# Performance work log

Measured on AMD Instinct MI355X. Metric: run time of the kernel, lower is better.

Reference implementation:

```python
import jax, jax.numpy as jnp
import numpy as np

N_HEAD = 16
D_K = 64


def _bn(x, g, b, eps=1e-5):
    # torch BatchNorm1d in training mode: biased batch variance
    m = jnp.mean(x, axis=0)
    v = jnp.var(x, axis=0)
    return (x - m) * jax.lax.rsqrt(v + eps) * g + b


def setup_inputs() -> dict:
    key = jax.random.key(0)
    ks = jax.random.split(key, 8)
    B, DX, NK, DKIN, H, DK, DO = 128, 1024, 1024, 512, N_HEAD, D_K, 512
    sc = 0.02
    return {
        "x": jax.random.normal(ks[0], (B, DX), dtype=jnp.float32),
        "k": jax.random.normal(ks[1], (B, NK, DKIN), dtype=jnp.float32),
        "bn1_g": jnp.ones((DX,), jnp.float32),
        "bn1_b": jnp.zeros((DX,), jnp.float32),
        "Wx": jax.random.normal(ks[2], (H * DK, DX), dtype=jnp.float32) * sc,
        "bx": jnp.zeros((H * DK,), jnp.float32),
        "Wk": jax.random.normal(ks[3], (H * DK, DKIN), dtype=jnp.float32) * sc,
        "bk": jnp.zeros((H * DK,), jnp.float32),
        "bn2_g": jnp.ones((DK,), jnp.float32),
        "bn2_b": jnp.zeros((DK,), jnp.float32),
        "Wlin": jax.random.normal(ks[4], (DK, DK), dtype=jnp.float32) * sc,
        "blin": jnp.zeros((DK,), jnp.float32),
        "Wo": jax.random.normal(ks[5], (DO, H * DK), dtype=jnp.float32) * sc,
        "bo": jnp.zeros((DO,), jnp.float32),
    }


def reference(x, k, bn1_g, bn1_b, Wx, bx, Wk, bk, bn2_g, bn2_b, Wlin, blin, Wo, bo):
    H, DK = N_HEAD, D_K
    B, DX = x.shape
    NK = k.shape[1]
    # outer BN + query projection (n_x == 1)
    xq = _bn(x, bn1_g, bn1_b) @ Wx.T + bx                     # (B, H*DK)
    xq = xq.reshape(B, H, DK).transpose(1, 0, 2).reshape(H * B, DK)
    kp = (k @ Wk.T + bk).reshape(B, NK, H, DK)
    kp = kp.transpose(2, 0, 1, 3).reshape(H * B, NK, DK)       # (H*B, NK, DK)
    # inner CrossAttention: BN + linear on the single query vector
    latent = _bn(xq, bn2_g, bn2_b) @ Wlin.T + blin             # (H*B, DK)
    u = jnp.einsum('bnd,bd->bn', kp, latent)                   # (H*B, NK)
    # softmax over the singleton query dim (dim=2) -> all ones, kept faithful
    attn = jax.nn.softmax(u[..., None], axis=-1)[..., 0]       # (H*B, NK)
    out = jnp.einsum('bnd,bn->bd', kp, attn)                   # (H*B, DK)
    out = out.reshape(H, B, DK).transpose(1, 0, 2).reshape(B, H * DK)
    x_hid = latent.reshape(H, B, DK).transpose(1, 0, 2).reshape(B, H * DK)
    # attn.view(n_head, batch, d_x_).permute(1,2,0).contiguous().view(batch, n_head, -1)
    attn_out = attn.reshape(H, B, NK).transpose(1, 2, 0).reshape(B, H, -1)
    return (attn_out, out @ Wo.T + bo, x_hid @ Wo.T + bo)
```

## Files before the change

### kernel.cpp

```cpp
#include <hip/hip_runtime.h>

typedef __attribute__((ext_vector_type(8))) short short8;
typedef __attribute__((ext_vector_type(4))) float floatx4;

__device__ __forceinline__ unsigned short f2bf(float f) {
    unsigned int x = __float_as_uint(f);
    x = x + 0x7FFFu + ((x >> 16) & 1u);
    return (unsigned short)(x >> 16);
}

template <typename OutT>
__device__ __forceinline__ void gemm_tile(
    const unsigned short* __restrict__ A, int lda,
    const unsigned short* __restrict__ B, int ldb,
    const float* __restrict__ bias, float bscale,
    OutT* __restrict__ C, int ldc, int tilesN, int K, int wave, int lane)
{
    int tm = wave / tilesN, tn = wave % tilesN;
    int mn = lane & 15, q = lane >> 4;
    const short8* ap = (const short8*)(A + (size_t)(tm * 16 + mn) * lda + q * 8);
    const short8* bp = (const short8*)(B + (size_t)(tn * 16 + mn) * ldb + q * 8);
    floatx4 acc = {0.f, 0.f, 0.f, 0.f};
    #pragma unroll 4
    for (int k = 0; k < K; k += 32) {
        short8 a = *ap; ap += 4;
        short8 b = *bp; bp += 4;
        acc = __builtin_amdgcn_mfma_f32_16x16x32_bf16(a, b, acc, 0, 0, 0);
    }
    int col = tn * 16 + mn;
    float bv = bias[col] * bscale;
    #pragma unroll
    for (int r = 0; r < 4; ++r) {
        int row = tm * 16 + q * 4 + r;
        float v = acc[r] + bv;
        OutT* dst = C + (size_t)row * ldc + col;
        if constexpr (sizeof(OutT) == 2) *dst = (OutT)f2bf(v);
        else                             *dst = (OutT)v;
    }
}

__global__ __launch_bounds__(256) void k_mega(
    const float* __restrict__ kk, float* __restrict__ part,
    const float* __restrict__ Wx, const float* __restrict__ Wk,
    const float* __restrict__ Wo, const float* __restrict__ Wl,
    unsigned short* __restrict__ Wxbf, unsigned short* __restrict__ Wkbf,
    unsigned short* __restrict__ Wobf, unsigned short* __restrict__ Wlbf,
    float4* __restrict__ attn_out,
    const float* __restrict__ x, const float* __restrict__ g1,
    const float* __restrict__ b1, unsigned short* __restrict__ xnbf)
{
    int blk = blockIdx.x, tid = threadIdx.x;
    if (blk < 1024) {
        int b = blk >> 3, c = blk & 7;
        int f4 = tid & 127;
        int rh = tid >> 7;
        const float4* base = (const float4*)kk
            + ((size_t)(b * 1024 + c * 128 + rh) * 128 + f4);
        float4 acc = {0.f, 0.f, 0.f, 0.f};
        #pragma unroll 8
        for (int it = 0; it < 64; ++it) {
            float4 v = base[(size_t)it * 256];
            acc.x += v.x; acc.y += v.y; acc.z += v.z; acc.w += v.w;
        }
        __shared__ float red[2][512];
        red[rh][f4 * 4 + 0] = acc.x;
        red[rh][f4 * 4 + 1] = acc.y;
        red[rh][f4 * 4 + 2] = acc.z;
        red[rh][f4 * 4 + 3] = acc.w;
        __syncthreads();
        for (int j = tid; j < 512; j += 256)
            part[((size_t)(c * 128 + b) << 9) + j] = red[0][j] + red[1][j];
    } else if (blk < 3076) {
        int f = (blk - 1024) * 256 + tid;
        const float* src; unsigned short* dst; int off;
        if (f < 262144)      { src = Wx; dst = Wxbf; off = f; }
        else if (f < 393216) { src = Wk; dst = Wkbf; off = f - 262144; }
        else if (f < 524288) { src = Wo; dst = Wobf; off = f - 393216; }
        else                 { src = Wl; dst = Wlbf; off = f - 524288; }
        float4 v = ((const float4*)src)[off];
        uint2 o;
        o.x = (unsigned int)f2bf(v.x) | ((unsigned int)f2bf(v.y) << 16);
        o.y = (unsigned int)f2bf(v.z) | ((unsigned int)f2bf(v.w) << 16);
        *(uint2*)(dst + off * 4) = o;
    } else if (blk < 5124) {
        int idx = (blk - 3076) * 256 + tid;
        float4 ones = {1.f, 1.f, 1.f, 1.f};
        attn_out[idx] = ones;
    } else {
        int c = (blk - 5124) * 256 + tid;
        float s = 0.f, ss = 0.f;
        #pragma unroll 8
        for (int b = 0; b < 128; ++b) {
            float v = x[b * 1024 + c];
            s += v; ss += v * v;
        }
        float m  = s * (1.f / 128.f);
        float va = ss * (1.f / 128.f) - m * m;
        float rs = rsqrtf(va + 1e-5f);
        float a  = rs * g1[c];
        float b2 = b1[c] - m * a;
        #pragma unroll 8
        for (int b = 0; b < 128; ++b)
            xnbf[b * 1024 + c] = f2bf(x[b * 1024 + c] * a + b2);
    }
}

__global__ __launch_bounds__(256) void k_combine_xq(
    const float* __restrict__ part, unsigned short* __restrict__ ksumbf,
    const unsigned short* __restrict__ xnbf, const unsigned short* __restrict__ Wxbf,
    const float* __restrict__ bx, float* __restrict__ xq)
{
    int blk = blockIdx.x, tid = threadIdx.x;
    if (blk < 32) {
        int idx = blk * 256 + tid;
        int b = idx >> 6;
        int j0 = (idx & 63) * 8;
        float s[8];
        #pragma unroll
        for (int u = 0; u < 8; ++u) s[u] = 0.f;
        #pragma unroll
        for (int c = 0; c < 8; ++c) {
            const float4* p = (const float4*)(part + ((size_t)(c * 128 + b) << 9) + j0);
            float4 a0 = p[0], a1 = p[1];
            s[0] += a0.x; s[1] += a0.y; s[2] += a0.z; s[3] += a0.w;
            s[4] += a1.x; s[5] += a1.y; s[6] += a1.z; s[7] += a1.w;
        }
        uint4 v;
        v.x = (unsigned int)f2bf(s[0]) | ((unsigned int)f2bf(s[1]) << 16);
        v.y = (unsigned int)f2bf(s[2]) | ((unsigned int)f2bf(s[3]) << 16);
        v.z = (unsigned int)f2bf(s[4]) | ((unsigned int)f2bf(s[5]) << 16);
        v.w = (unsigned int)f2bf(s[6]) | ((unsigned int)f2bf(s[7]) << 16);
        *(uint4*)(ksumbf + b * 512 + j0) = v;
    } else {
        int wave = ((blk - 32) * 256 + tid) >> 6;
        gemm_tile<float>(xnbf, 1024, Wxbf, 1024, bx, 1.f, xq, 1024, 64, 1024,
                         wave, tid & 63);
    }
}

__global__ __launch_bounds__(256) void k_bn2_outf(
    const float* __restrict__ xq, const float* __restrict__ g2,
    const float* __restrict__ b2, float* __restrict__ ab,
    const unsigned short* __restrict__ ksumbf, const unsigned short* __restrict__ Wkbf,
    const float* __restrict__ bk, unsigned short* __restrict__ concat)
{
    int blk = blockIdx.x, tid = threadIdx.x;
    if (blk < 64) {
        int d = blk;
        float s = 0.f, ss = 0.f;
        for (int e = tid; e < 2048; e += 256) {
            int b = e >> 4, h = e & 15;
            float v = xq[b * 1024 + h * 64 + d];
            s += v; ss += v * v;
        }
        __shared__ float r1[256], r2[256];
        r1[tid] = s; r2[tid] = ss;
        __syncthreads();
        for (int off = 128; off; off >>= 1) {
            if (tid < off) { r1[tid] += r1[tid + off]; r2[tid] += r2[tid + off]; }
            __syncthreads();
        }
        if (tid == 0) {
            float m  = r1[0] * (1.f / 2048.f);
            float va = r2[0] * (1.f / 2048.f) - m * m;
            float rs = rsqrtf(va + 1e-5f);
            float a  = rs * g2[d];
            ab[d] = a;
            ab[64 + d] = b2[d] - m * a;
        }
    } else {
        int wave = ((blk - 64) * 256 + tid) >> 6;
        gemm_tile<unsigned short>(ksumbf, 512, Wkbf, 512, bk, 1024.f, concat,
                                  1024, 64, 512, wave, tid & 63);
    }
}

__global__ __launch_bounds__(256) void k_latent(
    const float* __restrict__ xq, const float* __restrict__ ab,
    const unsigned short* __restrict__ Wlbf, const float* __restrict__ bl,
    unsigned short* __restrict__ xhid)
{
    int tid = threadIdx.x;
    int r = tid >> 6, dp = tid & 63;
    int row = blockIdx.x * 4 + r;
    int h = row >> 7, b = row & 127;
    __shared__ float xs[4][64];
    xs[r][dp] = xq[b * 1024 + h * 64 + dp] * ab[dp] + ab[64 + dp];
    __syncthreads();
    float dot = bl[dp];
    #pragma unroll 16
    for (int d = 0; d < 64; ++d)
        dot += xs[r][d] * __uint_as_float(((unsigned int)Wlbf[dp * 64 + d]) << 16);
    xhid[b * 1024 + h * 64 + dp] = f2bf(dot);
}

__global__ __launch_bounds__(256) void k_final_gemm(
    const unsigned short* __restrict__ concat, const unsigned short* __restrict__ Wobf,
    const float* __restrict__ bo, float* __restrict__ out12)
{
    int wave = (blockIdx.x * 256 + threadIdx.x) >> 6;
    gemm_tile<float>(concat, 1024, Wobf, 1024, bo, 1.f, out12, 512, 32, 1024,
                     wave, threadIdx.x & 63);
}

extern "C" void kernel_launch(void* const* d_in, const int* in_sizes, int n_in,
                              void* d_out, int out_size, void* d_ws, size_t ws_size,
                              hipStream_t stream) {
    (void)in_sizes; (void)n_in; (void)out_size; (void)ws_size;
    const float* x  = (const float*)d_in[0];
    const float* kk = (const float*)d_in[1];
    const float* g1 = (const float*)d_in[2];
    const float* b1 = (const float*)d_in[3];
    const float* Wx = (const float*)d_in[4];
    const float* bx = (const float*)d_in[5];
    const float* Wk = (const float*)d_in[6];
    const float* bk = (const float*)d_in[7];
    const float* g2 = (const float*)d_in[8];
    const float* b2 = (const float*)d_in[9];
    const float* Wl = (const float*)d_in[10];
    const float* bl = (const float*)d_in[11];
    const float* Wo = (const float*)d_in[12];
    const float* bo = (const float*)d_in[13];

    char* ws = (char*)d_ws;
    float*          part   = (float*)(ws + 0);
    unsigned short* Wxbf   = (unsigned short*)(ws + 2097152);
    unsigned short* Wkbf   = (unsigned short*)(ws + 4194304);
    unsigned short* Wobf   = (unsigned short*)(ws + 5242880);
    unsigned short* Wlbf   = (unsigned short*)(ws + 6291456);
    unsigned short* xnbf   = (unsigned short*)(ws + 6299648);
    unsigned short* ksumbf = (unsigned short*)(ws + 6561792);
    float*          xq     = (float*)(ws + 6692864);
    float*          ab     = (float*)(ws + 7217152);
    unsigned short* concat = (unsigned short*)(ws + 7217664);
    float*          out12  = (float*)d_out + 2097152;

    k_mega<<<5128, 256, 0, stream>>>(kk, part, Wx, Wk, Wo, Wl,
                                     Wxbf, Wkbf, Wobf, Wlbf,
                                     (float4*)d_out, x, g1, b1, xnbf);
    k_combine_xq<<<160, 256, 0, stream>>>(part, ksumbf, xnbf, Wxbf, bx, xq);
    k_bn2_outf<<<192, 256, 0, stream>>>(xq, g2, b2, ab, ksumbf, Wkbf, bk, concat);
    k_latent<<<512, 256, 0, stream>>>(xq, ab, Wlbf, bl, concat + 131072);
    k_final_gemm<<<128, 256, 0, stream>>>(concat, Wobf, bo, out12);
}
```

Baseline: 425.2 us.

## Fuse BN2 statistics into xq GEMM epilogue and merge latent MFMA with out-projection

The per-column BN2 sum and sum-of-squares are now accumulated with shared-memory and global atomics in the xq GEMM epilogue, which removes the separate reduction pass over xq. The latent linear layer moves onto MFMA and shares one launch with the Wk GEMM, so the pipeline has four launches instead of five. Block sizes drop to 128 threads with more blocks to spread the small GEMMs across more CUs. The cost is atomic contention and a float summation order that is no longer deterministic.

```diff
diff --git a/kernel.cpp b/kernel.cpp
--- a/kernel.cpp
+++ b/kernel.cpp
@@ -9,12 +9,13 @@
     return (unsigned short)(x >> 16);
 }
 
-template <typename OutT>
+template <typename OutT, bool STATS>
 __device__ __forceinline__ void gemm_tile(
     const unsigned short* __restrict__ A, int lda,
     const unsigned short* __restrict__ B, int ldb,
     const float* __restrict__ bias, float bscale,
-    OutT* __restrict__ C, int ldc, int tilesN, int K, int wave, int lane)
+    OutT* __restrict__ C, int ldc, int tilesN, int K, int wave, int lane,
+    float* sS, float* sSS)
 {
     int tm = wave / tilesN, tn = wave % tilesN;
     int mn = lane & 15, q = lane >> 4;
@@ -29,6 +30,7 @@
     }
     int col = tn * 16 + mn;
     float bv = bias[col] * bscale;
+    float lsum = 0.f, lss = 0.f;
     #pragma unroll
     for (int r = 0; r < 4; ++r) {
         int row = tm * 16 + q * 4 + r;
@@ -36,6 +38,12 @@
         OutT* dst = C + (size_t)row * ldc + col;
         if constexpr (sizeof(OutT) == 2) *dst = (OutT)f2bf(v);
         else                             *dst = (OutT)v;
+        if constexpr (STATS) { lsum += v; lss += v * v; }
+    }
+    if constexpr (STATS) {
+        int d = col & 63;
+        atomicAdd(&sS[d], lsum);
+        atomicAdd(&sSS[d], lss);
     }
 }
 
@@ -47,7 +55,8 @@
     unsigned short* __restrict__ Wobf, unsigned short* __restrict__ Wlbf,
     float4* __restrict__ attn_out,
     const float* __restrict__ x, const float* __restrict__ g1,
-    const float* __restrict__ b1, unsigned short* __restrict__ xnbf)
+    const float* __restrict__ b1, unsigned short* __restrict__ xnbf,
+    float* __restrict__ stats)
 {
     int blk = blockIdx.x, tid = threadIdx.x;
     if (blk < 1024) {
@@ -87,6 +96,7 @@
         float4 ones = {1.f, 1.f, 1.f, 1.f};
         attn_out[idx] = ones;
     } else {
+        if (blk == 5124 && tid < 128) stats[tid] = 0.f;
         int c = (blk - 5124) * 256 + tid;
         float s = 0.f, ss = 0.f;
         #pragma unroll 8
@@ -105,14 +115,15 @@
     }
 }
 
-__global__ __launch_bounds__(256) void k_combine_xq(
+__global__ __launch_bounds__(128) void k_combine_xq(
     const float* __restrict__ part, unsigned short* __restrict__ ksumbf,
     const unsigned short* __restrict__ xnbf, const unsigned short* __restrict__ Wxbf,
-    const float* __restrict__ bx, float* __restrict__ xq)
+    const float* __restrict__ bx, float* __restrict__ xq,
+    float* __restrict__ stats)
 {
     int blk = blockIdx.x, tid = threadIdx.x;
-    if (blk < 32) {
-        int idx = blk * 256 + tid;
+    if (blk < 64) {
+        int idx = blk * 128 + tid;
         int b = idx >> 6;
         int j0 = (idx & 63) * 8;
         float s[8];
@@ -132,75 +143,85 @@
         v.w = (unsigned int)f2bf(s[6]) | ((unsigned int)f2bf(s[7]) << 16);
         *(uint4*)(ksumbf + b * 512 + j0) = v;
     } else {
-        int wave = ((blk - 32) * 256 + tid) >> 6;
-        gemm_tile<float>(xnbf, 1024, Wxbf, 1024, bx, 1.f, xq, 1024, 64, 1024,
-                         wave, tid & 63);
-    }
-}
-
-__global__ __launch_bounds__(256) void k_bn2_outf(
-    const float* __restrict__ xq, const float* __restrict__ g2,
-    const float* __restrict__ b2, float* __restrict__ ab,
+        __shared__ float sS[64], sSS[64];
+        if (tid < 64) { sS[tid] = 0.f; sSS[tid] = 0.f; }
+        __syncthreads();
+        int wave = ((blk - 64) * 128 + tid) >> 6;
+        gemm_tile<float, true>(xnbf, 1024, Wxbf, 1024, bx, 1.f, xq, 1024, 64, 1024,
+                               wave, tid & 63, sS, sSS);
+        __syncthreads();
+        if (tid < 64)       atomicAdd(&stats[tid], sS[tid]);
+        else                atomicAdd(&stats[tid], sSS[tid - 64]);
+    }
+}
+
+__global__ __launch_bounds__(128) void k_outf_latent(
     const unsigned short* __restrict__ ksumbf, const unsigned short* __restrict__ Wkbf,
-    const float* __restrict__ bk, unsigned short* __restrict__ concat)
+    const float* __restrict__ bk,
+    const float* __restrict__ xq, const float* __restrict__ stats,
+    const float* __restrict__ g2, const float* __restrict__ b2g,
+    const unsigned short* __restrict__ Wlbf, const float* __restrict__ bl,
+    unsigned short* __restrict__ concat)
 {
     int blk = blockIdx.x, tid = threadIdx.x;
-    if (blk < 64) {
-        int d = blk;
-        float s = 0.f, ss = 0.f;
-        for (int e = tid; e < 2048; e += 256) {
-            int b = e >> 4, h = e & 15;
-            float v = xq[b * 1024 + h * 64 + d];
-            s += v; ss += v * v;
-        }
-        __shared__ float r1[256], r2[256];
-        r1[tid] = s; r2[tid] = ss;
-        __syncthreads();
-        for (int off = 128; off; off >>= 1) {
-            if (tid < off) { r1[tid] += r1[tid + off]; r2[tid] += r2[tid + off]; }
-            __syncthreads();
-        }
-        if (tid == 0) {
-            float m  = r1[0] * (1.f / 2048.f);
-            float va = r2[0] * (1.f / 2048.f) - m * m;
+    if (blk < 256) {
+        int wave = (blk * 128 + tid) >> 6;
+        gemm_tile<unsigned short, false>(ksumbf, 512, Wkbf, 512, bk, 1024.f,
+                                         concat, 1024, 64, 512, wave, tid & 63,
+                                         nullptr, nullptr);
+    } else {
+        __shared__ float sa[64], sb[64];
+        if (tid < 64) {
+            float s = stats[tid], ss = stats[64 + tid];
+            float m  = s * (1.f / 2048.f);
+            float va = ss * (1.f / 2048.f) - m * m;
             float rs = rsqrtf(va + 1e-5f);
-            float a  = rs * g2[d];
-            ab[d] = a;
-            ab[64 + d] = b2[d] - m * a;
-        }
-    } else {
-        int wave = ((blk - 64) * 256 + tid) >> 6;
-        gemm_tile<unsigned short>(ksumbf, 512, Wkbf, 512, bk, 1024.f, concat,
-                                  1024, 64, 512, wave, tid & 63);
-    }
-}
-
-__global__ __launch_bounds__(256) void k_latent(
-    const float* __restrict__ xq, const float* __restrict__ ab,
-    const unsigned short* __restrict__ Wlbf, const float* __restrict__ bl,
-    unsigned short* __restrict__ xhid)
-{
-    int tid = threadIdx.x;
-    int r = tid >> 6, dp = tid & 63;
-    int row = blockIdx.x * 4 + r;
-    int h = row >> 7, b = row & 127;
-    __shared__ float xs[4][64];
-    xs[r][dp] = xq[b * 1024 + h * 64 + dp] * ab[dp] + ab[64 + dp];
-    __syncthreads();
-    float dot = bl[dp];
-    #pragma unroll 16
-    for (int d = 0; d < 64; ++d)
-        dot += xs[r][d] * __uint_as_float(((unsigned int)Wlbf[dp * 64 + d]) << 16);
-    xhid[b * 1024 + h * 64 + dp] = f2bf(dot);
-}
-
-__global__ __launch_bounds__(256) void k_final_gemm(
+            float a  = rs * g2[tid];
+            sa[tid] = a;
+            sb[tid] = b2g[tid] - m * a;
+        }
+        __syncthreads();
+        int w = tid >> 6, lane = tid & 63;
+        int t = (blk - 256) * 2 + w;
+        int tm = t >> 2, tn = t & 3;
+        int mn = lane & 15, q = lane >> 4;
+        const float4* xp = (const float4*)(xq + (size_t)tm * 1024 + mn * 64 + q * 8);
+        const short8* bp = (const short8*)(Wlbf + (tn * 16 + mn) * 64 + q * 8);
+        floatx4 acc = {0.f, 0.f, 0.f, 0.f};
+        #pragma unroll
+        for (int kk = 0; kk < 2; ++kk) {
+            float4 x0 = xp[0], x1 = xp[1];
+            xp += 8;
+            int kb = kk * 32 + q * 8;
+            short8 af;
+            af[0] = (short)f2bf(x0.x * sa[kb + 0] + sb[kb + 0]);
+            af[1] = (short)f2bf(x0.y * sa[kb + 1] + sb[kb + 1]);
+            af[2] = (short)f2bf(x0.z * sa[kb + 2] + sb[kb + 2]);
+            af[3] = (short)f2bf(x0.w * sa[kb + 3] + sb[kb + 3]);
+            af[4] = (short)f2bf(x1.x * sa[kb + 4] + sb[kb + 4]);
+            af[5] = (short)f2bf(x1.y * sa[kb + 5] + sb[kb + 5]);
+            af[6] = (short)f2bf(x1.z * sa[kb + 6] + sb[kb + 6]);
+            af[7] = (short)f2bf(x1.w * sa[kb + 7] + sb[kb + 7]);
+            short8 bf = *bp; bp += 4;
+            acc = __builtin_amdgcn_mfma_f32_16x16x32_bf16(af, bf, acc, 0, 0, 0);
+        }
+        int d = tn * 16 + mn;
+        float bv = bl[d];
+        #pragma unroll
+        for (int r = 0; r < 4; ++r) {
+            int h = q * 4 + r;
+            concat[(size_t)(128 + tm) * 1024 + h * 64 + d] = f2bf(acc[r] + bv);
+        }
+    }
+}
+
+__global__ __launch_bounds__(128) void k_final_gemm(
     const unsigned short* __restrict__ concat, const unsigned short* __restrict__ Wobf,
     const float* __restrict__ bo, float* __restrict__ out12)
 {
-    int wave = (blockIdx.x * 256 + threadIdx.x) >> 6;
-    gemm_tile<float>(concat, 1024, Wobf, 1024, bo, 1.f, out12, 512, 32, 1024,
-                     wave, threadIdx.x & 63);
+    int wave = (blockIdx.x * 128 + threadIdx.x) >> 6;
+    gemm_tile<float, false>(concat, 1024, Wobf, 1024, bo, 1.f, out12, 512, 32, 1024,
+                            wave, threadIdx.x & 63, nullptr, nullptr);
 }
 
 extern "C" void kernel_launch(void* const* d_in, const int* in_sizes, int n_in,
@@ -231,15 +252,15 @@
     unsigned short* xnbf   = (unsigned short*)(ws + 6299648);
     unsigned short* ksumbf = (unsigned short*)(ws + 6561792);
     float*          xq     = (float*)(ws + 6692864);
-    float*          ab     = (float*)(ws + 7217152);
+    float*          stats  = (float*)(ws + 7217152);
     unsigned short* concat = (unsigned short*)(ws + 7217664);
     float*          out12  = (float*)d_out + 2097152;
 
     k_mega<<<5128, 256, 0, stream>>>(kk, part, Wx, Wk, Wo, Wl,
                                      Wxbf, Wkbf, Wobf, Wlbf,
-                                     (float4*)d_out, x, g1, b1, xnbf);
-    k_combine_xq<<<160, 256, 0, stream>>>(part, ksumbf, xnbf, Wxbf, bx, xq);
-    k_bn2_outf<<<192, 256, 0, stream>>>(xq, g2, b2, ab, ksumbf, Wkbf, bk, concat);
-    k_latent<<<512, 256, 0, stream>>>(xq, ab, Wlbf, bl, concat + 131072);
-    k_final_gemm<<<128, 256, 0, stream>>>(concat, Wobf, bo, out12);
-}
+                                     (float4*)d_out, x, g1, b1, xnbf, stats);
+    k_combine_xq<<<320, 128, 0, stream>>>(part, ksumbf, xnbf, Wxbf, bx, xq, stats);
+    k_outf_latent<<<512, 128, 0, stream>>>(ksumbf, Wkbf, bk, xq, stats,
+                                           g2, b2, Wlbf, bl, concat);
+    k_final_gemm<<<256, 128, 0, stream>>>(concat, Wobf, bo, out12);
+}
```

Measured after the change: 419.4 us (median of 2 runs). About the same (-1.3%).
